# Kernel optimization log

Hardware: AMD Instinct MI355X
Metric: run time of the kernel (lower is better)

## Reference

```python
import jax, jax.numpy as jnp
import numpy as np

N_NODES = 100000


def setup_inputs() -> dict:
    key = jax.random.key(0)
    k1, k2, k3, k4 = jax.random.split(key, 4)
    x = jax.random.normal(k1, (N_NODES, 128), dtype=jnp.float32)
    edge_index = jax.random.randint(k2, (2, 3200000), 0, N_NODES, dtype=jnp.int64)
    W = jax.random.normal(k3, (128, 16), dtype=jnp.float32) * 0.1
    b = jax.random.normal(k4, (16,), dtype=jnp.float32) * 0.1
    return {"x": x, "edge_index": edge_index, "W": W, "b": b}


def reference(x, edge_index, W, b):
    # GCNConv (PyG semantics): linear transform, add self-loops, symmetric
    # degree normalization, scatter-add aggregation; then relu + log_softmax.
    # Dropout uses training=self.training -> identity in eval mode.
    n = x.shape[0]
    h = x @ W  # [N, C]

    # add self-loops
    loop = jnp.arange(n, dtype=edge_index.dtype)
    row = jnp.concatenate([edge_index[0], loop])  # source
    col = jnp.concatenate([edge_index[1], loop])  # target

    # symmetric normalization: deg over targets (edge_weight = 1)
    ones = jnp.ones(row.shape[0], dtype=h.dtype)
    deg = jax.ops.segment_sum(ones, col, num_segments=n)
    deg_inv_sqrt = jnp.where(deg > 0, jax.lax.rsqrt(deg), 0.0)
    norm = deg_inv_sqrt[row] * deg_inv_sqrt[col]  # [E+N]

    # gather -> scale -> scatter-add at targets, then bias
    msgs = norm[:, None] * h[row]  # [E+N, C]
    out = jax.ops.segment_sum(msgs, col, num_segments=n) + b

    out = jax.nn.relu(out)
    return jax.nn.log_softmax(out, axis=1)
```

## Files before the change

### kernel.cpp

```cpp
#include <hip/hip_runtime.h>
#include <hip/hip_fp16.h>


typedef unsigned int u32;
typedef unsigned long long u64;

#define CPB_LOG 6
#define C1_LOG 11
#define SUBS 32
#define NB1_MAX 64
#define P1B 512
#define WCAP 192
#define P2SL 16
#define WPS (P1B / P2SL)
#define SUBCAP 208
#define TCAP (P2SL * SUBCAP)
#define LINB 196

__global__ __launch_bounds__(512) void lp1_kernel(const float* __restrict__ x,
                                                  const float* __restrict__ W,
                                                  const u32* __restrict__ ew,
                                                  __half* __restrict__ h16,
                                                  u32* __restrict__ cnt,
                                                  u32* __restrict__ wcur,
                                                  u32* __restrict__ binned1,
                                                  int N, int E, int NB1) {
    int blk = blockIdx.x;
    int t = threadIdx.x;
    if (blk < P1B) {
        __shared__ u32 wb[NB1_MAX];
        __shared__ int sflag;
        if (t < NB1_MAX) wb[t] = 0;
        if (t < 64) {
            u32 wv = ew[2 * t + 1];
            u64 mask = __ballot(wv != 0u);
            if (t == 0) sflag = (mask == 0ull) ? 1 : 0;
        }
        __syncthreads();
        int i64 = sflag;
        int chunk = (E + P1B - 1) / P1B;
        int cb = blk * chunk;
        int ce = min(cb + chunk, E);
        size_t wbase = (size_t)blk * NB1 * WCAP;
        if (i64) {
            const u64* ew64 = (const u64*)ew;
            for (int e = cb + t; e < ce; e += 512) {
                u32 r  = (u32)ew64[e];
                u32 cl = (u32)ew64[E + e];
                u32 c = cl >> C1_LOG;
                u32 pos = atomicAdd(&wb[c], 1u);
                if (pos < WCAP)
                    binned1[wbase + (size_t)c * WCAP + pos] = r | ((cl & ((1u << C1_LOG) - 1)) << 17);
            }
        } else {
            for (int e = cb + t; e < ce; e += 512) {
                u32 r  = ew[e];
                u32 cl = ew[E + e];
                u32 c = cl >> C1_LOG;
                u32 pos = atomicAdd(&wb[c], 1u);
                if (pos < WCAP)
                    binned1[wbase + (size_t)c * WCAP + pos] = r | ((cl & ((1u << C1_LOG) - 1)) << 17);
            }
        }
        __syncthreads();
        if (t < NB1) wcur[blk * NB1_MAX + t] = min(wb[t], (u32)WCAP);
    } else {
        int gid = (blk - P1B) * 512 + t;
        if (gid < N) cnt[gid] = 0u;
        int row = gid;
        if (row >= N) return;
        const float4* x4 = (const float4*)x;
        const float4* W4 = (const float4*)W;
        float acc[16];
#pragma unroll
        for (int c = 0; c < 16; ++c) acc[c] = 0.f;
        size_t xb = (size_t)row * 32;
#pragma unroll 2
        for (int chunk = 0; chunk < 32; ++chunk) {
            float4 xv = x4[xb + chunk];
            int k0 = chunk * 4;
            float xk[4] = { xv.x, xv.y, xv.z, xv.w };
#pragma unroll
            for (int q = 0; q < 4; ++q) {
                float4 w0 = W4[(k0 + q) * 4 + 0];
                float4 w1 = W4[(k0 + q) * 4 + 1];
                float4 w2 = W4[(k0 + q) * 4 + 2];
                float4 w3 = W4[(k0 + q) * 4 + 3];
                float xv_q = xk[q];
                acc[0]  = fmaf(xv_q, w0.x, acc[0]);
                acc[1]  = fmaf(xv_q, w0.y, acc[1]);
                acc[2]  = fmaf(xv_q, w0.z, acc[2]);
                acc[3]  = fmaf(xv_q, w0.w, acc[3]);
                acc[4]  = fmaf(xv_q, w1.x, acc[4]);
                acc[5]  = fmaf(xv_q, w1.y, acc[5]);
                acc[6]  = fmaf(xv_q, w1.z, acc[6]);
                acc[7]  = fmaf(xv_q, w1.w, acc[7]);
                acc[8]  = fmaf(xv_q, w2.x, acc[8]);
                acc[9]  = fmaf(xv_q, w2.y, acc[9]);
                acc[10] = fmaf(xv_q, w2.z, acc[10]);
                acc[11] = fmaf(xv_q, w2.w, acc[11]);
                acc[12] = fmaf(xv_q, w3.x, acc[12]);
                acc[13] = fmaf(xv_q, w3.y, acc[13]);
                acc[14] = fmaf(xv_q, w3.z, acc[14]);
                acc[15] = fmaf(xv_q, w3.w, acc[15]);
            }
        }
        union { __half2 h2; u32 u; } pk[8];
#pragma unroll
        for (int p = 0; p < 8; ++p) pk[p].h2 = __floats2half2_rn(acc[2 * p], acc[2 * p + 1]);
        uint4* orow = (uint4*)(h16 + (size_t)row * 16);
        orow[0] = make_uint4(pk[0].u, pk[1].u, pk[2].u, pk[3].u);
        orow[1] = make_uint4(pk[4].u, pk[5].u, pk[6].u, pk[7].u);
    }
}

__global__ __launch_bounds__(256) void pass2_kernel(const u32* __restrict__ binned1,
                                                    const u32* __restrict__ wcur,
                                                    u32* __restrict__ binned2,
                                                    u32* __restrict__ wlen,
                                                    u32* __restrict__ cnt,
                                                    int N, int NB1) {
    __shared__ u32 h2[1 << C1_LOG];
    __shared__ u32 scur[SUBS];
    int b = blockIdx.x;
    int c = b >> 4, sub = b & (P2SL - 1);
    int t = threadIdx.x;
    int l64 = t & 63, g = t >> 6;
    for (int i = t; i < (1 << C1_LOG); i += 256) h2[i] = 0;
    if (t < SUBS) scur[t] = 0;
    __syncthreads();
    for (int wg = 0; wg < WPS; wg += 4) {
        int pb = sub * WPS + wg + g;
        int len = (int)wcur[pb * NB1_MAX + c];
        const u32* win = &binned1[((size_t)pb * NB1 + c) * WCAP];
        for (int i = l64; i < len; i += 64) {
            u32 p = win[i];
            u32 lc = p >> 17;
            atomicAdd(&h2[lc], 1u);
            u32 s = lc >> CPB_LOG;
            u32 pos = atomicAdd(&scur[s], 1u);
            if (pos < SUBCAP)
                binned2[((size_t)(c * SUBS + s) * P2SL + sub) * SUBCAP + pos] = p & 0x7FFFFFu;
        }
    }
    __syncthreads();
    int colbase = c << C1_LOG;
    for (int i = t; i < (1 << C1_LOG); i += 256) {
        u32 v = h2[i];
        if (v && colbase + i < N) atomicAdd(&cnt[colbase + i], v);
    }
    if (t < SUBS)
        wlen[(size_t)(c * SUBS + t) * P2SL + sub] = min(scur[t], (u32)SUBCAP);
}

__global__ __launch_bounds__(256) void hs_kernel(const __half2* __restrict__ h16,
                                                 const u32* __restrict__ cnt,
                                                 __half2* __restrict__ hs2, int M2) {
    int i = blockIdx.x * 256 + threadIdx.x;
    if (i >= M2) return;
    float d = rsqrtf((float)cnt[i >> 3] + 1.0f);
    float2 hv = __half22float2(h16[i]);
    hs2[i] = __floats2half2_rn(hv.x * d, hv.y * d);
}

__global__ __launch_bounds__(256) void fgather_kernel(const u32* __restrict__ binned2,
                                                      const u32* __restrict__ wlen,
                                                      const u32* __restrict__ cnt,
                                                      const __half2* __restrict__ hs2,
                                                      const float* __restrict__ bias,
                                                      float* __restrict__ out, int N) {
    __shared__ u32 tile[TCAP];
    __shared__ u32 cbeg[65];
    __shared__ u32 cur[64];
    __shared__ u32 wln[P2SL];
    __shared__ u32 colNext;
    int b = blockIdx.x, t = threadIdx.x;
    int cbase = b << CPB_LOG;
    if (t < P2SL) wln[t] = wlen[(size_t)b * P2SL + t];
    if (t < 64) {
        int col = cbase + t;
        u32 v = (col < N) ? cnt[col] : 0u;
        u32 inc = v;
#pragma unroll
        for (int off = 1; off < 64; off <<= 1) {
            u32 o = __shfl_up(inc, off, 64);
            if (t >= off) inc += o;
        }
        cbeg[t] = inc - v;
        cur[t] = inc - v;
        if (t == 63) cbeg[64] = inc;
    }
    if (t == 0) colNext = 0;
    __syncthreads();
    int wv = t >> 6, lane = t & 63;
    const u32* fb = binned2 + (size_t)b * (P2SL * SUBCAP);
    for (int sub = wv; sub < P2SL; sub += 4) {
        int len = (int)wln[sub];
        const u32* sp = fb + sub * SUBCAP;
        for (int i = lane; i < len; i += 64) {
            u32 p = sp[i];
            u32 pos = atomicAdd(&cur[(p >> 17) & 63u], 1u);
            tile[pos] = p & 0x1FFFFu;
        }
    }
    __syncthreads();

    int l16 = t & 15;
    int c2 = l16 & 7, j = l16 >> 3;
    int leader = lane & 48;
    for (;;) {
        u32 mycol = 0;
        if (l16 == 0) mycol = atomicAdd(&colNext, 1u);
        mycol = __shfl(mycol, leader, 64);
        if (mycol >= 64u) break;
        int col = cbase + (int)mycol;
        if (col >= N) continue;
        u32 cs = cbeg[mycol], ce = cbeg[mycol + 1];
        float dt = rsqrtf((float)(ce - cs) + 1.0f);
        float ax = 0.f, ay = 0.f;
        u32 i = cs + j;
        for (; i + 14 < ce; i += 16) {
            u32 r0 = tile[i];
            u32 r1 = tile[i + 2];
            u32 r2 = tile[i + 4];
            u32 r3 = tile[i + 6];
            u32 r4 = tile[i + 8];
            u32 r5 = tile[i + 10];
            u32 r6 = tile[i + 12];
            u32 r7 = tile[i + 14];
            float2 v0 = __half22float2(hs2[(size_t)r0 * 8 + c2]);
            float2 v1 = __half22float2(hs2[(size_t)r1 * 8 + c2]);
            float2 v2 = __half22float2(hs2[(size_t)r2 * 8 + c2]);
            float2 v3 = __half22float2(hs2[(size_t)r3 * 8 + c2]);
            float2 v4 = __half22float2(hs2[(size_t)r4 * 8 + c2]);
            float2 v5 = __half22float2(hs2[(size_t)r5 * 8 + c2]);
            float2 v6 = __half22float2(hs2[(size_t)r6 * 8 + c2]);
            float2 v7 = __half22float2(hs2[(size_t)r7 * 8 + c2]);
            ax += ((v0.x + v1.x) + (v2.x + v3.x)) + ((v4.x + v5.x) + (v6.x + v7.x));
            ay += ((v0.y + v1.y) + (v2.y + v3.y)) + ((v4.y + v5.y) + (v6.y + v7.y));
        }
        for (; i < ce; i += 2) {
            u32 r = tile[i];
            float2 v = __half22float2(hs2[(size_t)r * 8 + c2]);
            ax += v.x; ay += v.y;
        }
        ax += __shfl_xor(ax, 8, 64);
        ay += __shfl_xor(ay, 8, 64);
        float2 sv = __half22float2(hs2[(size_t)col * 8 + c2]);
        float2 bb = ((const float2*)bias)[c2];
        float va = fmaxf(dt * (ax + sv.x) + bb.x, 0.f);
        float vb = fmaxf(dt * (ay + sv.y) + bb.y, 0.f);
        float m = fmaxf(va, vb);
#pragma unroll
        for (int off = 1; off < 8; off <<= 1) m = fmaxf(m, __shfl_xor(m, off, 64));
        float ss = expf(va - m) + expf(vb - m);
#pragma unroll
        for (int off = 1; off < 8; off <<= 1) ss += __shfl_xor(ss, off, 64);
        float ls = logf(ss);
        if (j == 0) {
            float2 o = { (va - m) - ls, (vb - m) - ls };
            ((float2*)(out + (size_t)col * 16))[c2] = o;
        }
    }
}

extern "C" void kernel_launch(void* const* d_in, const int* in_sizes, int n_in,
                              void* d_out, int out_size, void* d_ws, size_t ws_size,
                              hipStream_t stream) {
    const float* x  = (const float*)d_in[0];
    const u32*   ew = (const u32*)d_in[1];
    const float* W  = (const float*)d_in[2];
    const float* b  = (const float*)d_in[3];
    float* out = (float*)d_out;

    int N = in_sizes[0] / 128;
    int E = in_sizes[1] / 2;
    int NB  = (N + 63) >> CPB_LOG;
    int NB1 = (N + ((1 << C1_LOG) - 1)) >> C1_LOG;

    char* wsb = (char*)d_ws;
    size_t off = 0;
    auto alloc = [&](size_t sz) { void* p = wsb + off; off = (off + sz + 15) & ~(size_t)15; return p; };
    u32* cnt      = (u32*)alloc((size_t)N * 4);
    u32* wcur     = (u32*)alloc((size_t)P1B * NB1_MAX * 4);
    u32* wlen     = (u32*)alloc((size_t)NB1 * SUBS * P2SL * 4);
    __half* h16   = (__half*)alloc((size_t)N * 32);
    __half2* hs2  = (__half2*)alloc((size_t)N * 32);
    u32* binned1  = (u32*)alloc((size_t)P1B * NB1 * WCAP * 4);
    u32* binned2  = (u32*)alloc((size_t)NB1 * SUBS * P2SL * SUBCAP * 4);

    lp1_kernel<<<P1B + LINB, 512, 0, stream>>>(x, W, ew, h16, cnt, wcur, binned1, N, E, NB1);
    pass2_kernel<<<NB1 * P2SL, 256, 0, stream>>>(binned1, wcur, binned2, wlen, cnt, N, NB1);
    hs_kernel<<<(N * 8 + 255) / 256, 256, 0, stream>>>((const __half2*)h16, cnt, hs2, N * 8);
    fgather_kernel<<<NB, 256, 0, stream>>>(binned2, wlen, cnt, hs2, b, out, N);
}
```

Before: 81.14 us.

## Stage edge binning through shared-memory tiles to coalesce scattered global writes

```diff
diff --git a/kernel.cpp b/kernel.cpp
--- a/kernel.cpp
+++ b/kernel.cpp
@@ -16,6 +16,7 @@
 #define SUBCAP 208
 #define TCAP (P2SL * SUBCAP)
 #define LINB 196
+#define TILE 2048
 
 __global__ __launch_bounds__(512) void lp1_kernel(const float* __restrict__ x,
                                                   const float* __restrict__ W,
@@ -25,12 +26,18 @@
                                                   u32* __restrict__ wcur,
                                                   u32* __restrict__ binned1,
                                                   int N, int E, int NB1) {
+    __shared__ u32 tile[TILE];
+    __shared__ u32 dest[TILE];
+    __shared__ u32 hist[NB1_MAX];
+    __shared__ u32 sbase[NB1_MAX];
+    __shared__ u32 runb[NB1_MAX];
+    __shared__ u32 cur[NB1_MAX];
+    __shared__ u32 wloc[NB1_MAX];
+    __shared__ int sflag;
     int blk = blockIdx.x;
     int t = threadIdx.x;
     if (blk < P1B) {
-        __shared__ u32 wb[NB1_MAX];
-        __shared__ int sflag;
-        if (t < NB1_MAX) wb[t] = 0;
+        if (t < NB1_MAX) wloc[t] = 0;
         if (t < 64) {
             u32 wv = ew[2 * t + 1];
             u64 mask = __ballot(wv != 0u);
@@ -42,28 +49,58 @@
         int cb = blk * chunk;
         int ce = min(cb + chunk, E);
         size_t wbase = (size_t)blk * NB1 * WCAP;
-        if (i64) {
-            const u64* ew64 = (const u64*)ew;
-            for (int e = cb + t; e < ce; e += 512) {
-                u32 r  = (u32)ew64[e];
-                u32 cl = (u32)ew64[E + e];
-                u32 c = cl >> C1_LOG;
-                u32 pos = atomicAdd(&wb[c], 1u);
-                if (pos < WCAP)
-                    binned1[wbase + (size_t)c * WCAP + pos] = r | ((cl & ((1u << C1_LOG) - 1)) << 17);
+        const u64* ew64 = (const u64*)ew;
+        for (int tb = cb; tb < ce; tb += TILE) {
+            int tlen = min(TILE, ce - tb);
+            if (t < NB1_MAX) hist[t] = 0;
+            __syncthreads();
+            u32 p0 = 0, p1 = 0, p2 = 0, p3 = 0;
+            int c0 = -1, c1 = -1, c2 = -1, c3 = -1;
+            {
+                int e0 = tb + t;
+                int e1 = tb + 512 + t;
+                int e2 = tb + 1024 + t;
+                int e3 = tb + 1536 + t;
+                if (i64) {
+                    if (e0 < tb + tlen) { u32 r = (u32)ew64[e0], cl = (u32)ew64[E + e0]; c0 = cl >> C1_LOG; p0 = r | ((cl & 2047u) << 17); atomicAdd(&hist[c0], 1u); }
+                    if (e1 < tb + tlen) { u32 r = (u32)ew64[e1], cl = (u32)ew64[E + e1]; c1 = cl >> C1_LOG; p1 = r | ((cl & 2047u) << 17); atomicAdd(&hist[c1], 1u); }
+                    if (e2 < tb + tlen) { u32 r = (u32)ew64[e2], cl = (u32)ew64[E + e2]; c2 = cl >> C1_LOG; p2 = r | ((cl & 2047u) << 17); atomicAdd(&hist[c2], 1u); }
+                    if (e3 < tb + tlen) { u32 r = (u32)ew64[e3], cl = (u32)ew64[E + e3]; c3 = cl >> C1_LOG; p3 = r | ((cl & 2047u) << 17); atomicAdd(&hist[c3], 1u); }
+                } else {
+                    if (e0 < tb + tlen) { u32 r = ew[e0], cl = ew[E + e0]; c0 = cl >> C1_LOG; p0 = r | ((cl & 2047u) << 17); atomicAdd(&hist[c0], 1u); }
+                    if (e1 < tb + tlen) { u32 r = ew[e1], cl = ew[E + e1]; c1 = cl >> C1_LOG; p1 = r | ((cl & 2047u) << 17); atomicAdd(&hist[c1], 1u); }
+                    if (e2 < tb + tlen) { u32 r = ew[e2], cl = ew[E + e2]; c2 = cl >> C1_LOG; p2 = r | ((cl & 2047u) << 17); atomicAdd(&hist[c2], 1u); }
+                    if (e3 < tb + tlen) { u32 r = ew[e3], cl = ew[E + e3]; c3 = cl >> C1_LOG; p3 = r | ((cl & 2047u) << 17); atomicAdd(&hist[c3], 1u); }
+                }
             }
-        } else {
-            for (int e = cb + t; e < ce; e += 512) {
-                u32 r  = ew[e];
-                u32 cl = ew[E + e];
-                u32 c = cl >> C1_LOG;
-                u32 pos = atomicAdd(&wb[c], 1u);
-                if (pos < WCAP)
-                    binned1[wbase + (size_t)c * WCAP + pos] = r | ((cl & ((1u << C1_LOG) - 1)) << 17);
+            __syncthreads();
+            if (t < 64) {
+                u32 v = hist[t];
+                u32 inc = v;
+#pragma unroll
+                for (int off = 1; off < 64; off <<= 1) {
+                    u32 o = __shfl_up(inc, off, 64);
+                    if (t >= off) inc += o;
+                }
+                u32 excl = inc - v;
+                sbase[t] = excl;
+                cur[t] = excl;
+                runb[t] = wloc[t];
+                wloc[t] += v;
             }
-        }
-        __syncthreads();
-        if (t < NB1) wcur[blk * NB1_MAX + t] = min(wb[t], (u32)WCAP);
+            __syncthreads();
+            if (c0 >= 0) { u32 pos = atomicAdd(&cur[c0], 1u); u32 off = runb[c0] + (pos - sbase[c0]); dest[pos] = (off < WCAP) ? (u32)c0 * WCAP + off : 0xFFFFFFFFu; tile[pos] = p0; }
+            if (c1 >= 0) { u32 pos = atomicAdd(&cur[c1], 1u); u32 off = runb[c1] + (pos - sbase[c1]); dest[pos] = (off < WCAP) ? (u32)c1 * WCAP + off : 0xFFFFFFFFu; tile[pos] = p1; }
+            if (c2 >= 0) { u32 pos = atomicAdd(&cur[c2], 1u); u32 off = runb[c2] + (pos - sbase[c2]); dest[pos] = (off < WCAP) ? (u32)c2 * WCAP + off : 0xFFFFFFFFu; tile[pos] = p2; }
+            if (c3 >= 0) { u32 pos = atomicAdd(&cur[c3], 1u); u32 off = runb[c3] + (pos - sbase[c3]); dest[pos] = (off < WCAP) ? (u32)c3 * WCAP + off : 0xFFFFFFFFu; tile[pos] = p3; }
+            __syncthreads();
+            for (int i = t; i < tlen; i += 512) {
+                u32 d = dest[i];
+                if (d != 0xFFFFFFFFu) binned1[wbase + d] = tile[i];
+            }
+            __syncthreads();
+        }
+        if (t < NB1) wcur[blk * NB1_MAX + t] = min(wloc[t], (u32)WCAP);
     } else {
         int gid = (blk - P1B) * 512 + t;
         if (gid < N) cnt[gid] = 0u;
```

New measurement: 75.41 us. 7.1% less time.
